# Optimization experiments

Measured on AMD Instinct MI355X. Metric: run time of the kernel, lower is better.

Reference implementation:

```python
import jax, jax.numpy as jnp
import numpy as np

PSIZE = 3
PSTRIDE = 3
N = PSIZE * PSTRIDE   # 9 attention tokens
P = PSIZE ** 2        # 9 pixels per token


def setup_inputs() -> dict:
    key = jax.random.key(0)
    k1, k2, k3, k4, k5 = jax.random.split(key, 5)
    B, H, W, C = 8192, 9, 9, 256
    hidden = C // 2
    x = jax.random.normal(k1, (B, H, W, C), dtype=jnp.float32)
    W_fc = jax.random.normal(k2, (hidden, C), dtype=jnp.float32) * (C ** -0.5)
    b_fc = jax.random.normal(k3, (hidden,), dtype=jnp.float32) * 0.01
    block_idx = jax.random.randint(k4, (B,), 0, 1024, dtype=jnp.int32)
    match_vec = jax.random.randint(k5, (1024, 1), 0, 2, dtype=jnp.int32)
    return {"x": x, "W_fc": W_fc, "b_fc": b_fc, "block_idx": block_idx, "match_vec": match_vec}


def reference(x, W_fc, b_fc, block_idx, match_vec):
    B, H, Wd, C = x.shape
    hidden = W_fc.shape[0]
    scale = (hidden * P) ** -0.5

    # [B, pstride, psize, pstride, psize, C] -> patch-major [B, ps, ps, p, p, C]
    xv = x.reshape(B, PSTRIDE, PSIZE, PSTRIDE, PSIZE, C).transpose(0, 1, 3, 2, 4, 5)
    x_fc = xv.reshape(B, N, P, C)

    # linear projection C -> hidden, then flatten pixels: q [B, N, P*hidden]
    q = (jnp.einsum('bnpc,hc->bnph', x_fc, W_fc) + b_fc).reshape(B, N, P * hidden)

    attn = jnp.einsum('bnd,bmd->bnm', q, q) * scale  # [B, N, N]

    # additive mask: -100 on diagonal, zeroed out entirely for matched samples
    base = jnp.where(jnp.eye(N, dtype=bool), jnp.float32(-100.0), jnp.float32(0.0))
    cur_match = match_vec[block_idx].squeeze(-1)  # [B]
    mask = jnp.where(cur_match[:, None, None] == 1, jnp.float32(0.0), base[None])

    attn = jax.nn.softmax(attn + mask, axis=-1)

    v = xv.reshape(B, N, P * C)
    out = attn @ v  # [B, N, P*C]

    out = out.reshape(B, PSTRIDE, PSTRIDE, PSIZE, PSIZE, C)
    out = out.transpose(0, 1, 3, 2, 4, 5).reshape(B, H, Wd, C)
    return out
```

## Files before the change

### kernel.cpp

```cpp
#include <hip/hip_runtime.h>

typedef short short8 __attribute__((ext_vector_type(8)));
typedef float floatx16 __attribute__((ext_vector_type(16)));
typedef float floatx4 __attribute__((ext_vector_type(4)));

#define ROWS 81
#define CDIM 256
#define XT   0
#define QT   41472
#define SC   66048
#define AB   70144
#define TOT  70656

#define SWX(r) ((((r) & 15) << 4) ^ (((r) & 8) << 3))

__device__ __forceinline__ unsigned short f2bf(float f) {
    union { float f; unsigned int u; } v; v.f = f;
    return (unsigned short)((v.u + 0x7FFFu + ((v.u >> 16) & 1u)) >> 16);
}

__device__ __forceinline__ unsigned int cvtpk(float lo, float hi) {
    unsigned int r;
    asm("v_cvt_pk_bf16_f32 %0, %1, %2" : "=v"(r) : "v"(lo), "v"(hi));
    return r;
}

__global__ void wconv_kernel(const float* __restrict__ W,
                             unsigned short* __restrict__ Wb, int n) {
    int i = blockIdx.x * 256 + threadIdx.x;
    if (i < n) Wb[i] = f2bf(W[i]);
}

__device__ __forceinline__ void stage_store(char* smem, int k, float4 a0, float4 a1) {
    int gr = k >> 5;
    int c0 = (k & 31) * 8;
    int hh = gr / 9, ww = gr - hh * 9;
    int p = (hh % 3) * 3 + (ww % 3);
    int m = (hh / 3) * 3 + (ww / 3);
    int r = p * 9 + m;
    uint4 v;
    v.x = cvtpk(a0.x, a0.y);
    v.y = cvtpk(a0.z, a0.w);
    v.z = cvtpk(a1.x, a1.y);
    v.w = cvtpk(a1.z, a1.w);
    *(uint4*)(smem + XT + r * 512 + ((c0 * 2) ^ SWX(r))) = v;
}

__global__ __launch_bounds__(512, 2)
void attn_kernel(const float* __restrict__ x,
                 const unsigned short* __restrict__ Wb,
                 const float* __restrict__ b_fc,
                 const int* __restrict__ block_idx,
                 const int* __restrict__ match_vec,
                 float* __restrict__ out)
{
    __shared__ __align__(16) char smem[TOT];
    const int b     = blockIdx.x;
    const int t     = threadIdx.x;
    const int lane  = t & 63;
    const int wave  = t >> 6;
    const int l15   = lane & 15;
    const int kg    = lane >> 4;
    const int l31   = lane & 31;
    const int khalf = lane >> 5;

    int cm = 0;
    if (t < 9) cm = match_vec[block_idx[b]];

    const int rh = (wave & 1) * 48;
    const int hg = (wave >> 1) * 32;

    short8 wfrag[2][8];
#pragma unroll
    for (int s2 = 0; s2 < 2; ++s2) {
        const unsigned short* wr = Wb + (hg + s2 * 16 + l15) * CDIM + kg * 8;
#pragma unroll
        for (int ks = 0; ks < 8; ++ks)
            wfrag[s2][ks] = *(const short8*)(wr + ks * 32);
    }
    float bias2[2];
    bias2[0] = b_fc[hg + l15];
    bias2[1] = b_fc[hg + 16 + l15];

    {
        const float* xb = x + (size_t)b * (ROWS * CDIM);
        float4 a0[5], a1[5], t0, t1;
#pragma unroll
        for (int j = 0; j < 5; ++j) {
            int k = t + 512 * j;
            a0[j] = *(const float4*)(xb + k * 8);
            a1[j] = *(const float4*)(xb + k * 8 + 4);
        }
        const bool tail = (t < 32);
        if (tail) {
            t0 = *(const float4*)(xb + (2560 + t) * 8);
            t1 = *(const float4*)(xb + (2560 + t) * 8 + 4);
        }
#pragma unroll
        for (int j = 0; j < 5; ++j) stage_store(smem, t + 512 * j, a0[j], a1[j]);
        if (tail) stage_store(smem, 2560 + t, t0, t1);
    }
    __syncthreads();

    {
        floatx4 acc[3][2];
#pragma unroll
        for (int ii = 0; ii < 3; ++ii)
#pragma unroll
            for (int s2 = 0; s2 < 2; ++s2)
#pragma unroll
                for (int j = 0; j < 4; ++j) acc[ii][s2][j] = 0.f;
        __builtin_amdgcn_s_setprio(1);
#pragma unroll
        for (int ks = 0; ks < 8; ++ks) {
            int cb = ks * 64 + kg * 16;
#pragma unroll
            for (int tile = 0; tile < 3; ++tile) {
                int r = rh + tile * 16 + l15;
                short8 a = *(const short8*)(smem + XT + r * 512 + (cb ^ SWX(r)));
                acc[tile][0] = __builtin_amdgcn_mfma_f32_16x16x32_bf16(a, wfrag[0][ks], acc[tile][0], 0, 0, 0);
                acc[tile][1] = __builtin_amdgcn_mfma_f32_16x16x32_bf16(a, wfrag[1][ks], acc[tile][1], 0, 0, 0);
            }
        }
        __builtin_amdgcn_s_setprio(0);
#pragma unroll
        for (int tile = 0; tile < 3; ++tile)
#pragma unroll
            for (int s2 = 0; s2 < 2; ++s2) {
                int h2 = (hg + s2 * 16 + l15) * 2;
#pragma unroll
                for (int reg = 0; reg < 4; ++reg) {
                    int r = rh + tile * 16 + kg * 4 + reg;
                    *(unsigned short*)(smem + QT + r * 256 + (h2 ^ ((r & 15) << 4))) =
                        f2bf(acc[tile][s2][reg] + bias2[s2]);
                }
            }
    }
    __syncthreads();

    if (wave < 4) {
        floatx4 g;
#pragma unroll
        for (int ii = 0; ii < 4; ++ii) g[ii] = 0.f;
        int nc = (l15 < 9) ? l15 : 8;
#pragma unroll
        for (int s = 0; s < 9; ++s) {
            int ks = wave + s * 4;
            int kk = ks * 32 + kg * 8;
            int p  = kk >> 7;
            int h0 = (kk & 127) * 2;
            int row = p * 9 + nc;
            short8 f = *(const short8*)(smem + QT + row * 256 + (h0 ^ ((row & 15) << 4)));
            g = __builtin_amdgcn_mfma_f32_16x16x32_bf16(f, f, g, 0, 0, 0);
        }
        float* sc = (float*)(smem + SC + wave * 1024);
#pragma unroll
        for (int reg = 0; reg < 4; ++reg)
            sc[(kg * 4 + reg) * 16 + l15] = g[reg];
    }
    __syncthreads();

    if (t < 9) {
        const float scale = 0.029462782549439483f;
        const float* sc0 = (const float*)(smem + SC);
        const float* sc1 = (const float*)(smem + SC + 1024);
        const float* sc2 = (const float*)(smem + SC + 2048);
        const float* sc3 = (const float*)(smem + SC + 3072);
        float s[9];
        float mx = -1e30f;
#pragma unroll
        for (int m = 0; m < 9; ++m) {
            int o = t * 16 + m;
            float v = (sc0[o] + sc1[o] + sc2[o] + sc3[o]) * scale;
            if (m == t && cm != 1) v -= 100.f;
            s[m] = v;
            mx = fmaxf(mx, v);
        }
        float sum = 0.f;
#pragma unroll
        for (int m = 0; m < 9; ++m) { s[m] = __expf(s[m] - mx); sum += s[m]; }
        float inv = 1.f / sum;
        unsigned short* ab = (unsigned short*)(smem + AB) + t * 16;
#pragma unroll
        for (int m = 0; m < 9; ++m) ab[m] = f2bf(s[m] * inv);
#pragma unroll
        for (int m = 9; m < 16; ++m) ab[m] = 0;
    }
    __syncthreads();

    {
        const int n  = l31;
        const int nm = (n < 9) ? n : 0;
        short8 bf = *(const short8*)(smem + AB + nm * 32 + khalf * 16);
        floatx16 zero16;
#pragma unroll
        for (int ii = 0; ii < 16; ++ii) zero16[ii] = 0.f;
        float* ob = out + (size_t)b * (ROWS * CDIM);
        int nbase = 0;
        if (n < 9) nbase = ((n / 3) * 3) * 9 + (n % 3) * 3;
        const int c2 = (wave * 32 + l31) * 2;
#pragma unroll
        for (int pp = 0; pp < 9; ++pp) {
            short8 af;
#pragma unroll
            for (int j = 0; j < 8; ++j) {
                int mm = khalf ? 8 : j;
                int row = pp * 9 + mm;
                af[j] = *(const short*)(smem + XT + row * 512 + (c2 ^ SWX(row)));
            }
            floatx16 dacc = __builtin_amdgcn_mfma_f32_32x32x16_bf16(af, bf, zero16, 0, 0, 0);
            if (n < 9) {
                const int gr = nbase + (pp / 3) * 9 + (pp % 3);
#pragma unroll
                for (int q2 = 0; q2 < 4; ++q2) {
                    int c0 = wave * 32 + q2 * 8 + khalf * 4;
                    *(float4*)(ob + gr * CDIM + c0) =
                        make_float4(dacc[q2 * 4 + 0], dacc[q2 * 4 + 1],
                                    dacc[q2 * 4 + 2], dacc[q2 * 4 + 3]);
                }
            }
        }
    }
}

extern "C" void kernel_launch(void* const* d_in, const int* in_sizes, int n_in,
                              void* d_out, int out_size, void* d_ws, size_t ws_size,
                              hipStream_t stream) {
    const float* x    = (const float*)d_in[0];
    const float* W    = (const float*)d_in[1];
    const float* bfc  = (const float*)d_in[2];
    const int*   bidx = (const int*)d_in[3];
    const int*   mvec = (const int*)d_in[4];
    float* outp = (float*)d_out;
    unsigned short* Wb = (unsigned short*)d_ws;

    int nW = in_sizes[1];
    wconv_kernel<<<(nW + 255) / 256, 256, 0, stream>>>(W, Wb, nW);

    int B = in_sizes[0] / (ROWS * CDIM);
    attn_kernel<<<B, 512, 0, stream>>>(x, Wb, bfc, bidx, mvec, outp);
}
```

Baseline: 359.9 us.

## Compute full Gram and softmax redundantly per wave to remove two block barriers

Every wave now computes the full 9x9 Gram matrix itself (36 MFMAs instead of 9 split across 4 waves) and does the softmax in registers with cross-lane shuffles, writing its own attention weights to a per-wave shared slot. This removes the shared-memory score reduction, the single-thread softmax stage and two __syncthreads barriers. The cost is redundant MFMA work and extra LDS reads of Q in all 8 waves, and every thread now loads the match flag.

```diff
diff --git a/kernel.cpp b/kernel.cpp
--- a/kernel.cpp
+++ b/kernel.cpp
@@ -1,6 +1,7 @@
 #include <hip/hip_runtime.h>
 
 typedef short short8 __attribute__((ext_vector_type(8)));
+typedef short short4v __attribute__((ext_vector_type(4)));
 typedef float floatx16 __attribute__((ext_vector_type(16)));
 typedef float floatx4 __attribute__((ext_vector_type(4)));
 
@@ -8,9 +9,8 @@
 #define CDIM 256
 #define XT   0
 #define QT   41472
-#define SC   66048
-#define AB   70144
-#define TOT  70656
+#define AB   66048
+#define TOT  70144
 
 #define SWX(r) ((((r) & 15) << 4) ^ (((r) & 8) << 3))
 
@@ -64,8 +64,7 @@
     const int l31   = lane & 31;
     const int khalf = lane >> 5;
 
-    int cm = 0;
-    if (t < 9) cm = match_vec[block_idx[b]];
+    const int cm = match_vec[block_idx[b]];
 
     const int rh = (wave & 1) * 48;
     const int hg = (wave >> 1) * 32;
@@ -138,60 +137,58 @@
     }
     __syncthreads();
 
-    if (wave < 4) {
-        floatx4 g;
-#pragma unroll
-        for (int ii = 0; ii < 4; ++ii) g[ii] = 0.f;
-        int nc = (l15 < 9) ? l15 : 8;
+    char* slot = smem + AB + wave * 512;
+    {
+        floatx4 s0, s1, s2, s3;
+#pragma unroll
+        for (int ii = 0; ii < 4; ++ii) { s0[ii] = 0.f; s1[ii] = 0.f; s2[ii] = 0.f; s3[ii] = 0.f; }
+        const int nc = (l15 < 9) ? l15 : 8;
 #pragma unroll
         for (int s = 0; s < 9; ++s) {
-            int ks = wave + s * 4;
-            int kk = ks * 32 + kg * 8;
-            int p  = kk >> 7;
-            int h0 = (kk & 127) * 2;
-            int row = p * 9 + nc;
-            short8 f = *(const short8*)(smem + QT + row * 256 + (h0 ^ ((row & 15) << 4)));
-            g = __builtin_amdgcn_mfma_f32_16x16x32_bf16(f, f, g, 0, 0, 0);
-        }
-        float* sc = (float*)(smem + SC + wave * 1024);
-#pragma unroll
-        for (int reg = 0; reg < 4; ++reg)
-            sc[(kg * 4 + reg) * 16 + l15] = g[reg];
-    }
-    __syncthreads();
-
-    if (t < 9) {
+#pragma unroll
+            for (int ii = 0; ii < 4; ++ii) {
+                int ks = ii + s * 4;
+                int kk = ks * 32 + kg * 8;
+                int p  = kk >> 7;
+                int h0 = (kk & 127) * 2;
+                int row = p * 9 + nc;
+                short8 f = *(const short8*)(smem + QT + row * 256 + (h0 ^ ((row & 15) << 4)));
+                floatx4 tmp = __builtin_amdgcn_mfma_f32_16x16x32_bf16(
+                    f, f, (ii == 0 ? s0 : ii == 1 ? s1 : ii == 2 ? s2 : s3), 0, 0, 0);
+                if (ii == 0) s0 = tmp; else if (ii == 1) s1 = tmp; else if (ii == 2) s2 = tmp; else s3 = tmp;
+            }
+        }
+
         const float scale = 0.029462782549439483f;
-        const float* sc0 = (const float*)(smem + SC);
-        const float* sc1 = (const float*)(smem + SC + 1024);
-        const float* sc2 = (const float*)(smem + SC + 2048);
-        const float* sc3 = (const float*)(smem + SC + 3072);
-        float s[9];
-        float mx = -1e30f;
-#pragma unroll
-        for (int m = 0; m < 9; ++m) {
-            int o = t * 16 + m;
-            float v = (sc0[o] + sc1[o] + sc2[o] + sc3[o]) * scale;
-            if (m == t && cm != 1) v -= 100.f;
-            s[m] = v;
-            mx = fmaxf(mx, v);
-        }
-        float sum = 0.f;
-#pragma unroll
-        for (int m = 0; m < 9; ++m) { s[m] = __expf(s[m] - mx); sum += s[m]; }
+        float sv[4];
+#pragma unroll
+        for (int reg = 0; reg < 4; ++reg) {
+            int m = kg * 4 + reg;
+            float v = (s0[reg] + s1[reg] + s2[reg] + s3[reg]) * scale;
+            if (m == l15 && cm != 1) v -= 100.f;
+            sv[reg] = (m <= 8) ? v : -1e30f;
+        }
+        float mx = fmaxf(fmaxf(sv[0], sv[1]), fmaxf(sv[2], sv[3]));
+        mx = fmaxf(mx, __shfl_xor(mx, 16));
+        mx = fmaxf(mx, __shfl_xor(mx, 32));
+        float e0 = __expf(sv[0] - mx), e1 = __expf(sv[1] - mx);
+        float e2 = __expf(sv[2] - mx), e3 = __expf(sv[3] - mx);
+        float sum = e0 + e1 + e2 + e3;
+        sum += __shfl_xor(sum, 16);
+        sum += __shfl_xor(sum, 32);
         float inv = 1.f / sum;
-        unsigned short* ab = (unsigned short*)(smem + AB) + t * 16;
-#pragma unroll
-        for (int m = 0; m < 9; ++m) ab[m] = f2bf(s[m] * inv);
-#pragma unroll
-        for (int m = 9; m < 16; ++m) ab[m] = 0;
-    }
-    __syncthreads();
+        short4v aw;
+        aw[0] = (short)f2bf(e0 * inv);
+        aw[1] = (short)f2bf(e1 * inv);
+        aw[2] = (short)f2bf(e2 * inv);
+        aw[3] = (short)f2bf(e3 * inv);
+        *(short4v*)(slot + l15 * 32 + kg * 8) = aw;
+    }
 
     {
         const int n  = l31;
         const int nm = (n < 9) ? n : 0;
-        short8 bf = *(const short8*)(smem + AB + nm * 32 + khalf * 16);
+        short8 bf = *(const short8*)(slot + nm * 32 + khalf * 16);
         floatx16 zero16;
 #pragma unroll
         for (int ii = 0; ii < 16; ++ii) zero16[ii] = 0.f;
```

Measured after the change: 371.9 us. 3.3% more time.
